# Kernel optimization log

Measured on AMD Instinct MI355X. Metric: run time of the kernel, lower is better.

## Reference

```python
import jax, jax.numpy as jnp
import numpy as np

D = 8        # q_ndim (= dof_ndim)
HID = 200    # hidden_size
N = 16384    # batch of states
EPS = 0.1    # qdot regularizer coefficient in L()


def _lagrangian(z, Ws, bs):
    # z: (2D,) = [q, qdot]; angular_dims=() so CosSin is an identity pass-through
    v = z[D:]
    h = z
    for W, b in zip(Ws[:-1], bs[:-1]):
        h = jax.nn.softplus(h @ W + b)   # FCsoftplus blocks
    L = (h @ Ws[-1] + bs[-1])[0]          # final Linear -> scalar (Reshape(-1))
    return L + EPS * jnp.dot(v, v)


def setup_inputs():
    key = jax.random.key(0)
    ks = jax.random.split(key, 5)
    z = jax.random.normal(ks[0], (N, 2 * D), dtype=jnp.float32)
    t = jnp.zeros((), dtype=jnp.float32)

    def lin(k, fi, fo, scale):
        return (jax.random.normal(k, (fi, fo), dtype=jnp.float32)
                * jnp.float32(scale / np.sqrt(fi)))

    W0 = lin(ks[1], 2 * D, HID, 1.0)
    W1 = lin(ks[2], HID, HID, 1.0)
    W2 = lin(ks[3], HID, HID, 1.0)
    W3 = lin(ks[4], HID, 1, 0.01)  # small head keeps mass matrix M well conditioned
    b0 = jnp.zeros((HID,), jnp.float32)  # zero_bias init per FCsoftplus/Linear
    b1 = jnp.zeros((HID,), jnp.float32)
    b2 = jnp.zeros((HID,), jnp.float32)
    b3 = jnp.zeros((1,), jnp.float32)
    return dict(t=t, z=z, W0=W0, b0=b0, W1=W1, b1=b1, W2=W2, b2=b2, W3=W3, b3=b3)


def reference(t, z, W0, b0, W1, b1, W2, b2, W3, b3):
    # Euler-Lagrange dynamics (LagrangianDynamics):
    #   M a = dL/dq - (d2L/dq dv) v,  M = d2L/dv2;  dz/dt = [v, a]
    Ws = (W0, W1, W2, W3)
    bs = (b0, b1, b2, b3)
    Lfn = lambda zz: _lagrangian(zz, Ws, bs)

    def dyn_single(zi):
        g = jax.grad(Lfn)(zi)              # (2D,)  = [dL/dq, dL/dv]
        H = jax.jacfwd(jax.grad(Lfn))(zi)  # (2D,2D) Hessian of L wrt z
        v = zi[D:]
        M = H[D:, D:]                      # d(dL/dv)/dv  -> mass matrix
        C = H[D:, :D]                      # d(dL/dv)/dq
        F = g[:D] - C @ v
        a = jnp.linalg.solve(M, F)
        return jnp.concatenate([v, a])     # (2D,)

    return jax.vmap(dyn_single)(z)         # (N, 2D)
```

## Files before the change

kernel.cpp:

```cpp
#include <hip/hip_runtime.h>
#include <math.h>

#define DD 8
#define ZD 16
#define HID 200
#define EPSL 0.1f
#define BS 16
#define NTHREADS 1024
#define NKC 7
#define NMT 13
#define XSTR 216
#define CSTR 216
#define FBSTR 216
#define BSTR 208
#define WSTR 208
#define HSTR 20
#define NT4 4

#define KSC 1024.0f
#define SSC 64.0f
#define INV_K (1.0f/1024.0f)
#define INV_KS (1.0f/65536.0f)

typedef _Float16 half8 __attribute__((ext_vector_type(8)));
typedef _Float16 half4v __attribute__((ext_vector_type(4)));
typedef _Float16 half2v __attribute__((ext_vector_type(2)));
typedef float float4v __attribute__((ext_vector_type(4)));

#define S4 (NKC*NMT*64*8)
#define OFF_W1T 0
#define OFF_W2T (S4)
#define OFF_W1  (2*S4)
#define OFF_W2  (3*S4)
#define OFF_W0T (4*S4)
#define OFF_W0  (4*S4 + NMT*64*8)
#define WS_HALFS (4*S4 + NMT*64*8 + NKC*64*8)

#define CFSZ  (16*CSTR)
#define FBSZ  (16*FBSTR + 8)
#define O_XT  0
#define O_XB  (128*XSTR + 8)
#define O_CF  (2*(128*XSTR + 8))
#define O_U   (O_CF + 5*CFSZ)
#define O_FBA (O_U)
#define O_FBB (O_U + FBSZ)
#define O_GS  (O_U + 5120)
#define O_BSH (O_U + 2*FBSZ)
#define O_W0T (O_BSH + 3*BSTR)
#define SMEM_HALFS (O_W0T + 8*WSTR + 24)

__global__ void prep(const float* __restrict__ W0, const float* __restrict__ W1,
                     const float* __restrict__ W2, _Float16* __restrict__ ws)
{
    int idx = blockIdx.x * 256 + threadIdx.x;
    if (idx >= WS_HALFS) return;
    float v = 0.f;
    if (idx < 4*S4) {
        int arr = idx / S4, e = idx % S4;
        int kc = e / (NMT*64*8); int r = e % (NMT*64*8);
        int mt = r / (64*8); r %= 64*8;
        int lane = r / 8, j = r % 8;
        int m = mt*16 + (lane & 15);
        int k = kc*32 + (lane >> 4)*8 + j;
        if (m < HID && k < HID) {
            if      (arr == 0) v = W1[k*HID + m];
            else if (arr == 1) v = W2[k*HID + m];
            else if (arr == 2) v = W1[m*HID + k];
            else               v = W2[m*HID + k];
        }
    } else if (idx < OFF_W0) {
        int e = idx - OFF_W0T;
        int mt = e / (64*8); int r = e % (64*8);
        int lane = r / 8, j = r % 8;
        int m = mt*16 + (lane & 15);
        int k = (lane >> 4)*8 + j;
        if (m < HID && k < ZD) v = W0[k*HID + m];
    } else {
        int e = idx - OFF_W0;
        int kc = e / (64*8); int r = e % (64*8);
        int lane = r / 8, j = r % 8;
        int m = (lane & 15);
        int k = kc*32 + (lane >> 4)*8 + j;
        if (k < HID) v = W0[m*HID + k];
    }
    ws[idx] = (_Float16)v;
}

__device__ __forceinline__ half4v pk4(float4v a) {
    half2v lo = __builtin_bit_cast(half2v, __builtin_amdgcn_cvt_pkrtz(a.x, a.y));
    half2v hi = __builtin_bit_cast(half2v, __builtin_amdgcn_cvt_pkrtz(a.z, a.w));
    return __builtin_shufflevector(lo, hi, 0, 1, 2, 3);
}
__device__ __forceinline__ void sig_sp(float x, float& sp, float& sg) {
    float e = __expf(-fabsf(x));
    float r = 1.0f / (1.0f + e);
    sg = (x >= 0.f) ? r : (1.0f - r);
    sp = fmaxf(x, 0.f) + __logf(1.f + e);
}

__device__ __forceinline__ float4v run_fv(const half8* __restrict__ Asw,
                                          const _Float16* __restrict__ FBx,
                                          int fw, int lane, half8 pa)
{
    const int lm = lane & 15, q = lane >> 4;
    float4v acc = (float4v){0.f, 0.f, 0.f, 0.f};
    __builtin_amdgcn_s_setprio(1);
#pragma unroll
    for (int kc = 0; kc < NKC; ++kc) {
        half8 a = kc ? Asw[(kc*NMT + fw)*64 + lane] : pa;
        half8 x = *(const half8*)(FBx + lm*FBSTR + kc*32 + q*8);
        acc = __builtin_amdgcn_mfma_f32_16x16x32_f16(a, x, acc, 0, 0, 0);
    }
    __builtin_amdgcn_s_setprio(0);
    return acc;
}

template<int NT>
__device__ __forceinline__ void run_mvp(const half8* __restrict__ Asw,
                                        const _Float16* __restrict__ Xsrc,
                                        int mt0, int mtc, int lane,
                                        float4v acc[2][NT], half8 pa0, half8 pa1)
{
    const int lm = lane & 15, q = lane >> 4;
#pragma unroll
    for (int m = 0; m < 2; ++m)
#pragma unroll
        for (int n = 0; n < NT; ++n)
            acc[m][n] = (float4v){0.f, 0.f, 0.f, 0.f};
#pragma unroll
    for (int kc = 0; kc < NKC; ++kc) {
        half8 a0 = kc ? Asw[(kc*NMT + mt0)*64 + lane] : pa0;
        half8 a1 = pa1;
        if (kc && mtc > 1) a1 = Asw[(kc*NMT + mt0 + 1)*64 + lane];
        half8 x[NT];
#pragma unroll
        for (int n = 0; n < NT; ++n)
            x[n] = *(const half8*)(Xsrc + (n*16 + lm)*XSTR + kc*32 + q*8);
#pragma unroll
        for (int n = 0; n < NT; ++n)
            acc[0][n] = __builtin_amdgcn_mfma_f32_16x16x32_f16(a0, x[n], acc[0][n], 0, 0, 0);
        if (mtc > 1)
#pragma unroll
            for (int n = 0; n < NT; ++n)
                acc[1][n] = __builtin_amdgcn_mfma_f32_16x16x32_f16(a1, x[n], acc[1][n], 0, 0, 0);
    }
}

__global__ void __launch_bounds__(NTHREADS, 4)
lnn_main(const float* __restrict__ z,
         const float* __restrict__ W0, const float* __restrict__ b0,
         const float* __restrict__ b1, const float* __restrict__ b2,
         const float* __restrict__ W3,
         const _Float16* __restrict__ ws,
         float* __restrict__ out)
{
    __shared__ alignas(16) _Float16 smem[SMEM_HALFS];
    _Float16* const Xt  = smem + O_XT;
    _Float16* const Xb  = smem + O_XB;
    _Float16* const Cf  = smem + O_CF;
    _Float16* const FBa = smem + O_FBA;
    _Float16* const FBb = smem + O_FBB;
    _Float16* const bsh = smem + O_BSH;
    _Float16* const w0t = smem + O_W0T;
    float*    const gsh = (float*)(smem + O_GS);
    float*    const Hr  = (float*)(smem + O_U);

    const int tid  = threadIdx.x;
    const int wave = tid >> 6;
    const int lane = tid & 63;
    const int lm   = lane & 15;
    const int q    = lane >> 4;
    const int s0   = blockIdx.x * BS;

    const int twm  = wave >> 1;
    const int twn  = wave & 1;
    const int mt0t = (twm < 5) ? twm*2 : (twm + 5);
    const int mtct = (twm < 5) ? 2 : 1;

    const bool fok = (wave >= 3);
    const int  fw  = fok ? (wave - 3) : 0;
    const int  ubf = fw*16 + q*4;

    const half8* W1Tsw = (const half8*)(ws + OFF_W1T);
    const half8* W2Tsw = (const half8*)(ws + OFF_W2T);
    const half8* W1sw  = (const half8*)(ws + OFF_W1);
    const half8* W2sw  = (const half8*)(ws + OFF_W2);
    const half8* W0Tsw = (const half8*)(ws + OFF_W0T);
    const half8* W0sw  = (const half8*)(ws + OFF_W0);

    const half4v one = {(_Float16)1.f,(_Float16)1.f,(_Float16)1.f,(_Float16)1.f};

    float4v acc4[2][NT4];
    float4v accF;
    half8 pT0, pT1, pF;

    for (int idx = tid; idx < 128*16; idx += NTHREADS) {
        int r = idx >> 4, c = 200 + (idx & 15);
        Xt[r*XSTR + c] = (_Float16)0.f;
        Xb[r*XSTR + c] = (_Float16)0.f;
    }
    for (int idx = tid; idx < 2*16*16; idx += NTHREADS) {
        int buf = idx >> 8, r = (idx >> 4) & 15, c = 200 + (idx & 15);
        (buf ? FBb : FBa)[r*FBSTR + c] = (_Float16)0.f;
    }
    if (tid < 8) {
        Xt[128*XSTR + tid]  = (_Float16)0.f;
        Xb[128*XSTR + tid]  = (_Float16)0.f;
        FBa[16*FBSTR + tid] = (_Float16)0.f;
        FBb[16*FBSTR + tid] = (_Float16)0.f;
        Cf[1*CFSZ + tid]    = (_Float16)0.f;
    }
    for (int idx = tid; idx < 5*16*8; idx += NTHREADS) {
        int j = idx >> 7, r = (idx >> 3) & 15, c = 208 + (idx & 7);
        Cf[j*CFSZ + r*CSTR + c] = (_Float16)0.f;
    }
    for (int idx = tid; idx < 3*BSTR; idx += NTHREADS) {
        int l = idx / BSTR, u = idx % BSTR;
        float v = 0.f;
        if (u < HID) {
            if      (l == 0) v = b1[u];
            else if (l == 1) v = b2[u];
            else             v = KSC * W3[u];
        }
        bsh[idx] = (_Float16)v;
    }
    for (int idx = tid; idx < 8*WSTR + 24; idx += NTHREADS) {
        int t = idx / WSTR, u = idx % WSTR;
        w0t[idx] = (_Float16)((t < 8 && u < HID) ? SSC * W0[(DD + t)*HID + u] : 0.f);
    }
    if (fok) {
        half8 xz;
#pragma unroll
        for (int j = 0; j < 8; ++j) xz[j] = (_Float16)0.f;
        if (q < 2) {
            const float* zp = z + (size_t)(s0 + lm)*ZD + q*8;
#pragma unroll
            for (int j = 0; j < 8; ++j) xz[j] = (_Float16)zp[j];
        }
        float4v a0v = (float4v){0.f,0.f,0.f,0.f};
        half8 aw = W0Tsw[fw*64 + lane];
        a0v = __builtin_amdgcn_mfma_f32_16x16x32_f16(aw, xz, a0v, 0, 0, 0);
        float h[4], p[4];
#pragma unroll
        for (int r = 0; r < 4; ++r) {
            float bb = (ubf < HID) ? b0[ubf + r] : 0.f;
            float av = a0v[r] + bb;
            sig_sp(av, h[r], p[r]);
        }
        *(half4v*)(&FBa[lm*FBSTR + ubf])        = pk4((float4v){h[0],h[1],h[2],h[3]});
        *(half4v*)(&Cf[0*CFSZ + lm*CSTR + ubf]) = pk4((float4v){p[0],p[1],p[2],p[3]});
    }
    pT0 = W1Tsw[mt0t*64 + lane];
    pT1 = W1Tsw[(mt0t + mtct - 1)*64 + lane];
    pF  = W1Tsw[fw*64 + lane];
    __syncthreads();

    {
#pragma unroll
        for (int m = 0; m < 2; ++m)
#pragma unroll
            for (int n = 0; n < NT4; ++n)
                acc4[m][n] = (float4v){0.f, 0.f, 0.f, 0.f};
#pragma unroll
        for (int kc = 0; kc < NKC; ++kc) {
            half8 a0 = kc ? W1Tsw[(kc*NMT + mt0t)*64 + lane] : pT0;
            half8 a1 = pT1;
            if (kc && mtct > 1) a1 = W1Tsw[(kc*NMT + mt0t + 1)*64 + lane];
            half8 p0 = *(const half8*)(Cf + 0*CFSZ + lm*CSTR + kc*32 + q*8);
            half8 x[NT4];
#pragma unroll
            for (int n = 0; n < NT4; ++n) {
                half8 w0 = *(const half8*)(w0t + (twn*NT4 + n)*WSTR + kc*32 + q*8);
                x[n] = p0 * w0;
            }
#pragma unroll
            for (int n = 0; n < NT4; ++n)
                acc4[0][n] = __builtin_amdgcn_mfma_f32_16x16x32_f16(a0, x[n], acc4[0][n], 0, 0, 0);
            if (mtct > 1)
#pragma unroll
                for (int n = 0; n < NT4; ++n)
                    acc4[1][n] = __builtin_amdgcn_mfma_f32_16x16x32_f16(a1, x[n], acc4[1][n], 0, 0, 0);
        }
    }
    if (fok) {
        accF = run_fv(W1Tsw, FBa, fw, lane, pF);
        half4v bb = *(const half4v*)(&bsh[0*BSTR + ubf]);
        float h[4], p[4];
#pragma unroll
        for (int r = 0; r < 4; ++r) {
            float av = accF[r] + (float)bb[r];
            sig_sp(av, h[r], p[r]);
        }
        *(half4v*)(&FBb[lm*FBSTR + ubf])        = pk4((float4v){h[0],h[1],h[2],h[3]});
        *(half4v*)(&Cf[1*CFSZ + lm*CSTR + ubf]) = pk4((float4v){p[0],p[1],p[2],p[3]});
    }
    pF = W2Tsw[fw*64 + lane];
    __syncthreads();

    if (fok) {
        accF = run_fv(W2Tsw, FBb, fw, lane, pF);
        half4v bb = *(const half4v*)(&bsh[1*BSTR + ubf]);
        half4v w3 = *(const half4v*)(&bsh[2*BSTR + ubf]);
        float d2[4], c2[4];
#pragma unroll
        for (int r = 0; r < 4; ++r) {
            float av = accF[r] + (float)bb[r];
            float e = __expf(-fabsf(av));
            float rr = 1.f / (1.f + e);
            float sg = (av >= 0.f) ? rr : (1.f - rr);
            float wk = (float)w3[r];
            d2[r] = wk * sg;
            c2[r] = wk * sg * (1.f - sg);
        }
        *(half4v*)(&FBa[lm*FBSTR + ubf])        = pk4((float4v){d2[0],d2[1],d2[2],d2[3]});
        *(half4v*)(&Cf[2*CFSZ + lm*CSTR + ubf]) = pk4((float4v){c2[0],c2[1],c2[2],c2[3]});
    }
#pragma unroll
    for (int m = 0; m < 2; ++m)
        if (m < mtct) {
            const int ub = (mt0t + m)*16 + q*4;
            half4v p1 = *(const half4v*)(&Cf[1*CFSZ + lm*CSTR + ub]);
#pragma unroll
            for (int n = 0; n < NT4; ++n) {
                int row = (twn*NT4 + n)*16 + lm;
                *(half4v*)(&Xt[row*XSTR + ub]) = pk4(acc4[m][n]) * p1;
            }
        }
    pT0 = W2Tsw[mt0t*64 + lane];
    pT1 = W2Tsw[(mt0t + mtct - 1)*64 + lane];
    pF  = W2sw[fw*64 + lane];
    __syncthreads();

    run_mvp<NT4>(W2Tsw, Xt + twn*64*XSTR, mt0t, mtct, lane, acc4, pT0, pT1);
    if (fok) {
        accF = run_fv(W2sw, FBa, fw, lane, pF);
        half4v p1 = *(const half4v*)(&Cf[1*CFSZ + lm*CSTR + ubf]);
        half4v u1 = pk4(accF);
        *(half4v*)(&FBb[lm*FBSTR + ubf])        = u1 * p1;
        *(half4v*)(&Cf[3*CFSZ + lm*CSTR + ubf]) = u1 * (one - p1);
    }
    pF = W1sw[fw*64 + lane];
    __syncthreads();

    if (fok) {
        accF = run_fv(W1sw, FBb, fw, lane, pF);
        half4v p0 = *(const half4v*)(&Cf[0*CFSZ + lm*CSTR + ubf]);
        half4v u0 = pk4(accF);
        half4v d0 = u0 * p0;
        *(half4v*)(&FBa[lm*FBSTR + ubf])        = d0;
        *(half4v*)(&Cf[4*CFSZ + lm*CSTR + ubf]) = d0 * (one - p0);
    }
#pragma unroll
    for (int m = 0; m < 2; ++m)
        if (m < mtct) {
            const int ub = (mt0t + m)*16 + q*4;
            half4v c2 = *(const half4v*)(&Cf[2*CFSZ + lm*CSTR + ub]);
#pragma unroll
            for (int n = 0; n < NT4; ++n) {
                int row = (twn*NT4 + n)*16 + lm;
                *(half4v*)(&Xb[row*XSTR + ub]) = pk4(acc4[m][n]) * c2;
            }
        }
    pT0 = W2sw[mt0t*64 + lane];
    pT1 = W2sw[(mt0t + mtct - 1)*64 + lane];
    if (wave == 14) pF = W0sw[lane];
    __syncthreads();

    run_mvp<NT4>(W2sw, Xb + twn*64*XSTR, mt0t, mtct, lane, acc4, pT0, pT1);
    if (wave == 14) {
        float4v g = (float4v){0.f,0.f,0.f,0.f};
        __builtin_amdgcn_s_setprio(1);
#pragma unroll
        for (int kc = 0; kc < NKC; ++kc) {
            half8 a = kc ? W0sw[kc*64 + lane] : pF;
            half8 x = *(const half8*)(FBa + lm*FBSTR + kc*32 + q*8);
            g = __builtin_amdgcn_mfma_f32_16x16x32_f16(a, x, g, 0, 0, 0);
        }
        __builtin_amdgcn_s_setprio(0);
        if (q < 2) {
            float4v gv;
            gv.x = g.x*INV_K; gv.y = g.y*INV_K; gv.z = g.z*INV_K; gv.w = g.w*INV_K;
            *(float4v*)(&gsh[lm*8 + q*4]) = gv;
        }
    }
#pragma unroll
    for (int m = 0; m < 2; ++m)
        if (m < mtct) {
            const int ub = (mt0t + m)*16 + q*4;
            half4v p1 = *(const half4v*)(&Cf[1*CFSZ + lm*CSTR + ub]);
            half4v c3 = *(const half4v*)(&Cf[3*CFSZ + lm*CSTR + ub]);
#pragma unroll
            for (int n = 0; n < NT4; ++n) {
                int row = (twn*NT4 + n)*16 + lm;
                half4v th1 = *(const half4v*)(&Xt[row*XSTR + ub]);
                *(half4v*)(&Xt[row*XSTR + ub]) = pk4(acc4[m][n]) * p1 + c3 * th1;
            }
        }
    pT0 = W1sw[mt0t*64 + lane];
    pT1 = W1sw[(mt0t + mtct - 1)*64 + lane];
    __syncthreads();

    run_mvp<NT4>(W1sw, Xt + twn*64*XSTR, mt0t, mtct, lane, acc4, pT0, pT1);
#pragma unroll
    for (int m = 0; m < 2; ++m)
        if (m < mtct) {
            const int ub = (mt0t + m)*16 + q*4;
            half4v p0 = *(const half4v*)(&Cf[0*CFSZ + lm*CSTR + ub]);
            half4v c4 = *(const half4v*)(&Cf[4*CFSZ + lm*CSTR + ub]);
#pragma unroll
            for (int n = 0; n < NT4; ++n) {
                int row = (twn*NT4 + n)*16 + lm;
                half4v w0 = *(const half4v*)(&w0t[(twn*NT4 + n)*WSTR + ub]);
                *(half4v*)(&Xb[row*XSTR + ub]) = pk4(acc4[m][n]) * p0 + c4 * w0;
            }
        }
    if (wave < 8) pF = W0sw[lane];
    __syncthreads();

    if (wave < 8) {
        float4v hacc = (float4v){0.f,0.f,0.f,0.f};
#pragma unroll
        for (int kc = 0; kc < NKC; ++kc) {
            half8 a = kc ? W0sw[kc*64 + lane] : pF;
            half8 x = *(const half8*)(Xb + (wave*16 + lm)*XSTR + kc*32 + q*8);
            hacc = __builtin_amdgcn_mfma_f32_16x16x32_f16(a, x, hacc, 0, 0, 0);
        }
        int row = wave*16 + lm;
        float4v hv;
        hv.x = hacc.x*INV_KS; hv.y = hacc.y*INV_KS;
        hv.z = hacc.z*INV_KS; hv.w = hacc.w*INV_KS;
        *(float4v*)(&Hr[row*HSTR + q*4]) = hv;
    }
    __syncthreads();

    if (tid < BS) {
        const int s = tid;
        float M[DD][DD], F[DD], v[DD], a[DD];
#pragma unroll
        for (int c = 0; c < DD; ++c) v[c] = z[(s0 + s)*ZD + DD + c];
#pragma unroll
        for (int r = 0; r < DD; ++r) {
            float f = gsh[s*8 + r];
#pragma unroll
            for (int c = 0; c < DD; ++c) {
                M[r][c] = Hr[(r*16 + s)*HSTR + DD + c] + ((r == c) ? 2.f*EPSL : 0.f);
                f -= Hr[(r*16 + s)*HSTR + c] * v[c];
            }
            F[r] = f;
        }
#pragma unroll
        for (int col = 0; col < DD; ++col) {
            const float inv = 1.f / M[col][col];
#pragma unroll
            for (int r = col + 1; r < DD; ++r) {
                const float fac = M[r][col] * inv;
#pragma unroll
                for (int c = col + 1; c < DD; ++c) M[r][c] -= fac * M[col][c];
                F[r] -= fac * F[col];
            }
        }
#pragma unroll
        for (int r = DD - 1; r >= 0; --r) {
            float ssum = F[r];
#pragma unroll
            for (int c = r + 1; c < DD; ++c) ssum -= M[r][c] * a[c];
            a[r] = ssum / M[r][r];
        }
        float* op = out + (size_t)(s0 + s)*ZD;
#pragma unroll
        for (int c = 0; c < DD; ++c) { op[c] = v[c]; op[DD + c] = a[c]; }
    }
}

extern "C" void kernel_launch(void* const* d_in, const int* in_sizes, int n_in,
                              void* d_out, int out_size, void* d_ws, size_t ws_size,
                              hipStream_t stream)
{
    const float* z  = (const float*)d_in[1];
    const float* W0 = (const float*)d_in[2];
    const float* b0 = (const float*)d_in[3];
    const float* W1 = (const float*)d_in[4];
    const float* b1 = (const float*)d_in[5];
    const float* W2 = (const float*)d_in[6];
    const float* b2 = (const float*)d_in[7];
    const float* W3 = (const float*)d_in[8];
    float* out = (float*)d_out;
    _Float16* ws = (_Float16*)d_ws;

    const int n = in_sizes[1] / (2*DD);

    prep<<<dim3((WS_HALFS + 255)/256), dim3(256), 0, stream>>>(W0, W1, W2, ws);
    lnn_main<<<dim3(n / BS), dim3(NTHREADS), 0, stream>>>(
        z, W0, b0, b1, b2, W3, ws, out);
}
```

Before: 151.5 us.

## Halve block to 8 waves with 4-M-tile per-wave work and prefetched weights

Reduces the block from 16 to 8 waves and reassigns work so each wave handles up to 4 M-tiles of the tangent matmuls, and all waves share the forward-vector chain with up to 2 tiles each. The weight fragments for the next K chunk are now software-prefetched inside the loop instead of preloading the first chunk before each barrier. This aims to raise per-wave A-fragment reuse and cut barrier/wave overhead, at the cost of more registers per thread (occupancy bound lowered to 2 blocks) and less latency hiding from fewer waves.

```diff
diff --git a/kernel.cpp b/kernel.cpp
--- a/kernel.cpp
+++ b/kernel.cpp
@@ -6,7 +6,7 @@
 #define HID 200
 #define EPSL 0.1f
 #define BS 16
-#define NTHREADS 1024
+#define NTHREADS 512
 #define NKC 7
 #define NMT 13
 #define XSTR 216
@@ -98,55 +98,69 @@
     sp = fmaxf(x, 0.f) + __logf(1.f + e);
 }
 
-__device__ __forceinline__ float4v run_fv(const half8* __restrict__ Asw,
-                                          const _Float16* __restrict__ FBx,
-                                          int fw, int lane, half8 pa)
+__device__ __forceinline__ void run_fv2(const half8* __restrict__ Asw,
+                                        const _Float16* __restrict__ FBx,
+                                        int ff0, int ffc, int lane, half8 pa,
+                                        float4v accF[2])
 {
     const int lm = lane & 15, q = lane >> 4;
-    float4v acc = (float4v){0.f, 0.f, 0.f, 0.f};
+    accF[0] = (float4v){0.f,0.f,0.f,0.f};
+    accF[1] = (float4v){0.f,0.f,0.f,0.f};
     __builtin_amdgcn_s_setprio(1);
 #pragma unroll
     for (int kc = 0; kc < NKC; ++kc) {
-        half8 a = kc ? Asw[(kc*NMT + fw)*64 + lane] : pa;
+        half8 a0 = kc ? Asw[(kc*NMT + ff0)*64 + lane] : pa;
         half8 x = *(const half8*)(FBx + lm*FBSTR + kc*32 + q*8);
-        acc = __builtin_amdgcn_mfma_f32_16x16x32_f16(a, x, acc, 0, 0, 0);
+        accF[0] = __builtin_amdgcn_mfma_f32_16x16x32_f16(a0, x, accF[0], 0, 0, 0);
+        if (ffc > 1) {
+            half8 a1 = Asw[(kc*NMT + ff0 + 1)*64 + lane];
+            accF[1] = __builtin_amdgcn_mfma_f32_16x16x32_f16(a1, x, accF[1], 0, 0, 0);
+        }
     }
     __builtin_amdgcn_s_setprio(0);
-    return acc;
 }
 
 template<int NT>
-__device__ __forceinline__ void run_mvp(const half8* __restrict__ Asw,
+__device__ __forceinline__ void run_mv4(const half8* __restrict__ Asw,
                                         const _Float16* __restrict__ Xsrc,
                                         int mt0, int mtc, int lane,
-                                        float4v acc[2][NT], half8 pa0, half8 pa1)
+                                        float4v acc[4][NT])
 {
     const int lm = lane & 15, q = lane >> 4;
-#pragma unroll
-    for (int m = 0; m < 2; ++m)
+    half8 ac[4], an[4];
+#pragma unroll
+    for (int m = 0; m < 4; ++m)
+        if (m < mtc) ac[m] = Asw[(mt0 + m)*64 + lane];
+#pragma unroll
+    for (int m = 0; m < 4; ++m)
 #pragma unroll
         for (int n = 0; n < NT; ++n)
             acc[m][n] = (float4v){0.f, 0.f, 0.f, 0.f};
 #pragma unroll
     for (int kc = 0; kc < NKC; ++kc) {
-        half8 a0 = kc ? Asw[(kc*NMT + mt0)*64 + lane] : pa0;
-        half8 a1 = pa1;
-        if (kc && mtc > 1) a1 = Asw[(kc*NMT + mt0 + 1)*64 + lane];
+        if (kc + 1 < NKC) {
+#pragma unroll
+            for (int m = 0; m < 4; ++m)
+                if (m < mtc) an[m] = Asw[((kc+1)*NMT + mt0 + m)*64 + lane];
+        }
         half8 x[NT];
 #pragma unroll
         for (int n = 0; n < NT; ++n)
             x[n] = *(const half8*)(Xsrc + (n*16 + lm)*XSTR + kc*32 + q*8);
 #pragma unroll
-        for (int n = 0; n < NT; ++n)
-            acc[0][n] = __builtin_amdgcn_mfma_f32_16x16x32_f16(a0, x[n], acc[0][n], 0, 0, 0);
-        if (mtc > 1)
-#pragma unroll
-            for (int n = 0; n < NT; ++n)
-                acc[1][n] = __builtin_amdgcn_mfma_f32_16x16x32_f16(a1, x[n], acc[1][n], 0, 0, 0);
-    }
-}
-
-__global__ void __launch_bounds__(NTHREADS, 4)
+        for (int m = 0; m < 4; ++m)
+            if (m < mtc)
+#pragma unroll
+                for (int n = 0; n < NT; ++n)
+                    acc[m][n] = __builtin_amdgcn_mfma_f32_16x16x32_f16(ac[m], x[n], acc[m][n], 0, 0, 0);
+        if (kc + 1 < NKC) {
+#pragma unroll
+            for (int m = 0; m < 4; ++m) ac[m] = an[m];
+        }
+    }
+}
+
+__global__ void __launch_bounds__(NTHREADS, 2)
 lnn_main(const float* __restrict__ z,
          const float* __restrict__ W0, const float* __restrict__ b0,
          const float* __restrict__ b1, const float* __restrict__ b2,
@@ -172,14 +186,15 @@
     const int q    = lane >> 4;
     const int s0   = blockIdx.x * BS;
 
-    const int twm  = wave >> 1;
+    const int mg   = wave >> 1;
     const int twn  = wave & 1;
-    const int mt0t = (twm < 5) ? twm*2 : (twm + 5);
-    const int mtct = (twm < 5) ? 2 : 1;
-
-    const bool fok = (wave >= 3);
-    const int  fw  = fok ? (wave - 3) : 0;
-    const int  ubf = fw*16 + q*4;
+    const int mt0t = (mg == 0) ? 0 : (1 + 3*mg);
+    const int mtct = (mg == 0) ? 4 : 3;
+
+    const int ffc = (wave == 0 || wave == 1 || wave == 4) ? 1 : 2;
+    const int ff0 = (wave == 0) ? 0 : (wave == 1) ? 1 : (wave == 4) ? 2 :
+                    (wave == 2) ? 3 : (wave == 3) ? 5 : (wave == 5) ? 7 :
+                    (wave == 6) ? 9 : 11;
 
     const half8* W1Tsw = (const half8*)(ws + OFF_W1T);
     const half8* W2Tsw = (const half8*)(ws + OFF_W2T);
@@ -190,9 +205,9 @@
 
     const half4v one = {(_Float16)1.f,(_Float16)1.f,(_Float16)1.f,(_Float16)1.f};
 
-    float4v acc4[2][NT4];
-    float4v accF;
-    half8 pT0, pT1, pF;
+    float4v acc4[4][NT4];
+    float4v accF[2];
+    half8 pF;
 
     for (int idx = tid; idx < 128*16; idx += NTHREADS) {
         int r = idx >> 4, c = 200 + (idx & 15);
@@ -228,7 +243,7 @@
         int t = idx / WSTR, u = idx % WSTR;
         w0t[idx] = (_Float16)((t < 8 && u < HID) ? SSC * W0[(DD + t)*HID + u] : 0.f);
     }
-    if (fok) {
+    {
         half8 xz;
 #pragma unroll
         for (int j = 0; j < 8; ++j) xz[j] = (_Float16)0.f;
@@ -237,35 +252,44 @@
 #pragma unroll
             for (int j = 0; j < 8; ++j) xz[j] = (_Float16)zp[j];
         }
-        float4v a0v = (float4v){0.f,0.f,0.f,0.f};
-        half8 aw = W0Tsw[fw*64 + lane];
-        a0v = __builtin_amdgcn_mfma_f32_16x16x32_f16(aw, xz, a0v, 0, 0, 0);
-        float h[4], p[4];
-#pragma unroll
-        for (int r = 0; r < 4; ++r) {
-            float bb = (ubf < HID) ? b0[ubf + r] : 0.f;
-            float av = a0v[r] + bb;
-            sig_sp(av, h[r], p[r]);
-        }
-        *(half4v*)(&FBa[lm*FBSTR + ubf])        = pk4((float4v){h[0],h[1],h[2],h[3]});
-        *(half4v*)(&Cf[0*CFSZ + lm*CSTR + ubf]) = pk4((float4v){p[0],p[1],p[2],p[3]});
-    }
-    pT0 = W1Tsw[mt0t*64 + lane];
-    pT1 = W1Tsw[(mt0t + mtct - 1)*64 + lane];
-    pF  = W1Tsw[fw*64 + lane];
-    __syncthreads();
-
-    {
-#pragma unroll
-        for (int m = 0; m < 2; ++m)
+#pragma unroll
+        for (int f = 0; f < 2; ++f)
+            if (f < ffc) {
+                float4v a0v = (float4v){0.f,0.f,0.f,0.f};
+                half8 aw = W0Tsw[(ff0 + f)*64 + lane];
+                a0v = __builtin_amdgcn_mfma_f32_16x16x32_f16(aw, xz, a0v, 0, 0, 0);
+                const int ub = (ff0 + f)*16 + q*4;
+                float h[4], p[4];
+#pragma unroll
+                for (int r = 0; r < 4; ++r) {
+                    float bb = (ub < HID) ? b0[ub + r] : 0.f;
+                    float av = a0v[r] + bb;
+                    sig_sp(av, h[r], p[r]);
+                }
+                if (ub < 200) *(half4v*)(&FBa[lm*FBSTR + ub]) = pk4((float4v){h[0],h[1],h[2],h[3]});
+                *(half4v*)(&Cf[0*CFSZ + lm*CSTR + ub]) = pk4((float4v){p[0],p[1],p[2],p[3]});
+            }
+    }
+    pF = W1Tsw[ff0*64 + lane];
+    __syncthreads();
+
+    {
+        half8 ac[4], an[4];
+#pragma unroll
+        for (int m = 0; m < 4; ++m)
+            if (m < mtct) ac[m] = W1Tsw[(mt0t + m)*64 + lane];
+#pragma unroll
+        for (int m = 0; m < 4; ++m)
 #pragma unroll
             for (int n = 0; n < NT4; ++n)
                 acc4[m][n] = (float4v){0.f, 0.f, 0.f, 0.f};
 #pragma unroll
         for (int kc = 0; kc < NKC; ++kc) {
-            half8 a0 = kc ? W1Tsw[(kc*NMT + mt0t)*64 + lane] : pT0;
-            half8 a1 = pT1;
-            if (kc && mtct > 1) a1 = W1Tsw[(kc*NMT + mt0t + 1)*64 + lane];
+            if (kc + 1 < NKC) {
+#pragma unroll
+                for (int m = 0; m < 4; ++m)
+                    if (m < mtct) an[m] = W1Tsw[((kc+1)*NMT + mt0t + m)*64 + lane];
+            }
             half8 p0 = *(const half8*)(Cf + 0*CFSZ + lm*CSTR + kc*32 + q*8);
             half8 x[NT4];
 #pragma unroll
@@ -274,49 +298,62 @@
                 x[n] = p0 * w0;
             }
 #pragma unroll
-            for (int n = 0; n < NT4; ++n)
-                acc4[0][n] = __builtin_amdgcn_mfma_f32_16x16x32_f16(a0, x[n], acc4[0][n], 0, 0, 0);
-            if (mtct > 1)
-#pragma unroll
-                for (int n = 0; n < NT4; ++n)
-                    acc4[1][n] = __builtin_amdgcn_mfma_f32_16x16x32_f16(a1, x[n], acc4[1][n], 0, 0, 0);
-        }
-    }
-    if (fok) {
-        accF = run_fv(W1Tsw, FBa, fw, lane, pF);
-        half4v bb = *(const half4v*)(&bsh[0*BSTR + ubf]);
-        float h[4], p[4];
-#pragma unroll
-        for (int r = 0; r < 4; ++r) {
-            float av = accF[r] + (float)bb[r];
-            sig_sp(av, h[r], p[r]);
-        }
-        *(half4v*)(&FBb[lm*FBSTR + ubf])        = pk4((float4v){h[0],h[1],h[2],h[3]});
-        *(half4v*)(&Cf[1*CFSZ + lm*CSTR + ubf]) = pk4((float4v){p[0],p[1],p[2],p[3]});
-    }
-    pF = W2Tsw[fw*64 + lane];
-    __syncthreads();
-
-    if (fok) {
-        accF = run_fv(W2Tsw, FBb, fw, lane, pF);
-        half4v bb = *(const half4v*)(&bsh[1*BSTR + ubf]);
-        half4v w3 = *(const half4v*)(&bsh[2*BSTR + ubf]);
-        float d2[4], c2[4];
-#pragma unroll
-        for (int r = 0; r < 4; ++r) {
-            float av = accF[r] + (float)bb[r];
-            float e = __expf(-fabsf(av));
-            float rr = 1.f / (1.f + e);
-            float sg = (av >= 0.f) ? rr : (1.f - rr);
-            float wk = (float)w3[r];
-            d2[r] = wk * sg;
-            c2[r] = wk * sg * (1.f - sg);
-        }
-        *(half4v*)(&FBa[lm*FBSTR + ubf])        = pk4((float4v){d2[0],d2[1],d2[2],d2[3]});
-        *(half4v*)(&Cf[2*CFSZ + lm*CSTR + ubf]) = pk4((float4v){c2[0],c2[1],c2[2],c2[3]});
-    }
-#pragma unroll
-    for (int m = 0; m < 2; ++m)
+            for (int m = 0; m < 4; ++m)
+                if (m < mtct)
+#pragma unroll
+                    for (int n = 0; n < NT4; ++n)
+                        acc4[m][n] = __builtin_amdgcn_mfma_f32_16x16x32_f16(ac[m], x[n], acc4[m][n], 0, 0, 0);
+            if (kc + 1 < NKC) {
+#pragma unroll
+                for (int m = 0; m < 4; ++m) ac[m] = an[m];
+            }
+        }
+    }
+    {
+        run_fv2(W1Tsw, FBa, ff0, ffc, lane, pF, accF);
+#pragma unroll
+        for (int f = 0; f < 2; ++f)
+            if (f < ffc) {
+                const int ub = (ff0 + f)*16 + q*4;
+                half4v bb = *(const half4v*)(&bsh[0*BSTR + ub]);
+                float h[4], p[4];
+#pragma unroll
+                for (int r = 0; r < 4; ++r) {
+                    float av = accF[f][r] + (float)bb[r];
+                    sig_sp(av, h[r], p[r]);
+                }
+                if (ub < 200) *(half4v*)(&FBb[lm*FBSTR + ub]) = pk4((float4v){h[0],h[1],h[2],h[3]});
+                *(half4v*)(&Cf[1*CFSZ + lm*CSTR + ub]) = pk4((float4v){p[0],p[1],p[2],p[3]});
+            }
+    }
+    pF = W2Tsw[ff0*64 + lane];
+    __syncthreads();
+
+    {
+        run_fv2(W2Tsw, FBb, ff0, ffc, lane, pF, accF);
+#pragma unroll
+        for (int f = 0; f < 2; ++f)
+            if (f < ffc) {
+                const int ub = (ff0 + f)*16 + q*4;
+                half4v bb = *(const half4v*)(&bsh[1*BSTR + ub]);
+                half4v w3 = *(const half4v*)(&bsh[2*BSTR + ub]);
+                float d2[4], c2[4];
+#pragma unroll
+                for (int r = 0; r < 4; ++r) {
+                    float av = accF[f][r] + (float)bb[r];
+                    float e = __expf(-fabsf(av));
+                    float rr = 1.f / (1.f + e);
+                    float sg = (av >= 0.f) ? rr : (1.f - rr);
+                    float wk = (float)w3[r];
+                    d2[r] = wk * sg;
+                    c2[r] = wk * sg * (1.f - sg);
+                }
+                if (ub < 200) *(half4v*)(&FBa[lm*FBSTR + ub]) = pk4((float4v){d2[0],d2[1],d2[2],d2[3]});
+                *(half4v*)(&Cf[2*CFSZ + lm*CSTR + ub]) = pk4((float4v){c2[0],c2[1],c2[2],c2[3]});
+            }
+    }
+#pragma unroll
+    for (int m = 0; m < 4; ++m)
         if (m < mtct) {
             const int ub = (mt0t + m)*16 + q*4;
             half4v p1 = *(const half4v*)(&Cf[1*CFSZ + lm*CSTR + ub]);
@@ -326,32 +363,40 @@
                 *(half4v*)(&Xt[row*XSTR + ub]) = pk4(acc4[m][n]) * p1;
             }
         }
-    pT0 = W2Tsw[mt0t*64 + lane];
-    pT1 = W2Tsw[(mt0t + mtct - 1)*64 + lane];
-    pF  = W2sw[fw*64 + lane];
-    __syncthreads();
-
-    run_mvp<NT4>(W2Tsw, Xt + twn*64*XSTR, mt0t, mtct, lane, acc4, pT0, pT1);
-    if (fok) {
-        accF = run_fv(W2sw, FBa, fw, lane, pF);
-        half4v p1 = *(const half4v*)(&Cf[1*CFSZ + lm*CSTR + ubf]);
-        half4v u1 = pk4(accF);
-        *(half4v*)(&FBb[lm*FBSTR + ubf])        = u1 * p1;
-        *(half4v*)(&Cf[3*CFSZ + lm*CSTR + ubf]) = u1 * (one - p1);
-    }
-    pF = W1sw[fw*64 + lane];
-    __syncthreads();
-
-    if (fok) {
-        accF = run_fv(W1sw, FBb, fw, lane, pF);
-        half4v p0 = *(const half4v*)(&Cf[0*CFSZ + lm*CSTR + ubf]);
-        half4v u0 = pk4(accF);
-        half4v d0 = u0 * p0;
-        *(half4v*)(&FBa[lm*FBSTR + ubf])        = d0;
-        *(half4v*)(&Cf[4*CFSZ + lm*CSTR + ubf]) = d0 * (one - p0);
-    }
-#pragma unroll
-    for (int m = 0; m < 2; ++m)
+    pF = W2sw[ff0*64 + lane];
+    __syncthreads();
+
+    run_mv4<NT4>(W2Tsw, Xt + twn*64*XSTR, mt0t, mtct, lane, acc4);
+    {
+        run_fv2(W2sw, FBa, ff0, ffc, lane, pF, accF);
+#pragma unroll
+        for (int f = 0; f < 2; ++f)
+            if (f < ffc) {
+                const int ub = (ff0 + f)*16 + q*4;
+                half4v p1 = *(const half4v*)(&Cf[1*CFSZ + lm*CSTR + ub]);
+                half4v u1 = pk4(accF[f]);
+                if (ub < 200) *(half4v*)(&FBb[lm*FBSTR + ub]) = u1 * p1;
+                *(half4v*)(&Cf[3*CFSZ + lm*CSTR + ub]) = u1 * (one - p1);
+            }
+    }
+    pF = W1sw[ff0*64 + lane];
+    __syncthreads();
+
+    {
+        run_fv2(W1sw, FBb, ff0, ffc, lane, pF, accF);
+#pragma unroll
+        for (int f = 0; f < 2; ++f)
+            if (f < ffc) {
+                const int ub = (ff0 + f)*16 + q*4;
+                half4v p0 = *(const half4v*)(&Cf[0*CFSZ + lm*CSTR + ub]);
+                half4v u0 = pk4(accF[f]);
+                half4v d0 = u0 * p0;
+                if (ub < 200) *(half4v*)(&FBa[lm*FBSTR + ub]) = d0;
+                *(half4v*)(&Cf[4*CFSZ + lm*CSTR + ub]) = d0 * (one - p0);
+            }
+    }
+#pragma unroll
+    for (int m = 0; m < 4; ++m)
         if (m < mtct) {
             const int ub = (mt0t + m)*16 + q*4;
             half4v c2 = *(const half4v*)(&Cf[2*CFSZ + lm*CSTR + ub]);
@@ -361,13 +406,11 @@
                 *(half4v*)(&Xb[row*XSTR + ub]) = pk4(acc4[m][n]) * c2;
             }
         }
-    pT0 = W2sw[mt0t*64 + lane];
-    pT1 = W2sw[(mt0t + mtct - 1)*64 + lane];
-    if (wave == 14) pF = W0sw[lane];
-    __syncthreads();
-
-    run_mvp<NT4>(W2sw, Xb + twn*64*XSTR, mt0t, mtct, lane, acc4, pT0, pT1);
-    if (wave == 14) {
+    if (wave == 7) pF = W0sw[lane];
+    __syncthreads();
+
+    run_mv4<NT4>(W2sw, Xb + twn*64*XSTR, mt0t, mtct, lane, acc4);
+    if (wave == 7) {
         float4v g = (float4v){0.f,0.f,0.f,0.f};
         __builtin_amdgcn_s_setprio(1);
 #pragma unroll
@@ -384,7 +427,7 @@
         }
     }
 #pragma unroll
-    for (int m = 0; m < 2; ++m)
+    for (int m = 0; m < 4; ++m)
         if (m < mtct) {
             const int ub = (mt0t + m)*16 + q*4;
             half4v p1 = *(const half4v*)(&Cf[1*CFSZ + lm*CSTR + ub]);
@@ -396,13 +439,11 @@
                 *(half4v*)(&Xt[row*XSTR + ub]) = pk4(acc4[m][n]) * p1 + c3 * th1;
             }
         }
-    pT0 = W1sw[mt0t*64 + lane];
-    pT1 = W1sw[(mt0t + mtct - 1)*64 + lane];
-    __syncthreads();
-
-    run_mvp<NT4>(W1sw, Xt + twn*64*XSTR, mt0t, mtct, lane, acc4, pT0, pT1);
-#pragma unroll
-    for (int m = 0; m < 2; ++m)
+    __syncthreads();
+
+    run_mv4<NT4>(W1sw, Xt + twn*64*XSTR, mt0t, mtct, lane, acc4);
+#pragma unroll
+    for (int m = 0; m < 4; ++m)
         if (m < mtct) {
             const int ub = (mt0t + m)*16 + q*4;
             half4v p0 = *(const half4v*)(&Cf[0*CFSZ + lm*CSTR + ub]);
@@ -414,10 +455,10 @@
                 *(half4v*)(&Xb[row*XSTR + ub]) = pk4(acc4[m][n]) * p0 + c4 * w0;
             }
         }
-    if (wave < 8) pF = W0sw[lane];
-    __syncthreads();
-
-    if (wave < 8) {
+    pF = W0sw[lane];
+    __syncthreads();
+
+    {
         float4v hacc = (float4v){0.f,0.f,0.f,0.f};
 #pragma unroll
         for (int kc = 0; kc < NKC; ++kc) {
```

Result: slower. 178.5 us (+17.8%).
